# Kernel tuning notes

Hardware: AMD Instinct MI355X
Metric: run time of the kernel (lower is better)

Reference implementation:

```python
import jax, jax.numpy as jnp
import numpy as np

B, P, T, H, M = 32, 64, 256, 128, 16
MEAS_E, MOT_E = 64, 64
E = MEAS_E + MOT_E  # total_emb = 128
MAP_SIZE, MAP_EMB = 18, 128
ALPHA = 0.5  # soft-resampling alpha
OUT_DIM = 32 * 9 * 9  # encode output: conv1 stride2 18->9, conv2/3 stride1


def setup_inputs() -> dict:
    key = jax.random.key(0)
    ks = jax.random.split(key, 24)
    def g(i, shape, scale=0.05):
        return jax.random.normal(ks[i], shape, dtype=jnp.float32) * scale
    return {
        "map_in": jax.random.normal(ks[0], (B, 1, MAP_SIZE, MAP_SIZE), dtype=jnp.float32),
        "measurement_in": jax.random.normal(ks[1], (B, T, M), dtype=jnp.float32),
        "motion_in": jax.random.normal(ks[2], (B, T, 3), dtype=jnp.float32),
        "h0": jax.random.uniform(ks[3], (B * P, H), dtype=jnp.float32),
        "eps": jax.random.normal(ks[4], (T, B * P, H), dtype=jnp.float32),
        "u": jax.random.uniform(ks[5], (T, B, P), dtype=jnp.float32),
        "conv1_w": g(6, (16, 1, 5, 5)),
        "conv2_w": g(7, (32, 16, 3, 3)),
        "conv3_w": g(8, (32, 32, 3, 3)),
        "W_mapemb": g(9, (OUT_DIM, MAP_EMB)), "b_mapemb": jnp.zeros((MAP_EMB,), jnp.float32),
        "W_m2meas": g(10, (MAP_EMB, MEAS_E)), "b_m2meas": jnp.zeros((MEAS_E,), jnp.float32),
        "W_m2mot": g(11, (MAP_EMB, MOT_E)), "b_m2mot": jnp.zeros((MOT_E,), jnp.float32),
        "W_meas": g(12, (M, MEAS_E)), "b_meas": jnp.zeros((MEAS_E,), jnp.float32),
        "W_mot": g(13, (3, MOT_E)), "b_mot": jnp.zeros((MOT_E,), jnp.float32),
        "Wz": g(14, (H + E, H)), "bz": jnp.zeros((H,), jnp.float32),
        "Wr": g(15, (H + E, H)), "br": jnp.zeros((H,), jnp.float32),
        "Wn": g(16, (H + E, 2 * H)), "bn": jnp.zeros((2 * H,), jnp.float32),
        "Wo": g(17, (H + E, 1)), "bo": jnp.zeros((1,), jnp.float32),
        "W_label": g(18, (H, 3)), "b_label": jnp.zeros((3,), jnp.float32),
    }


def _encode(map_in, c1, c2, c3):
    # Conv -> ReLU -> BatchNorm(eval: identity w/ default stats) -> Dropout(eval: identity)
    dn = ("NCHW", "OIHW", "NCHW")
    x = jax.lax.conv_general_dilated(map_in, c1, (2, 2), [(2, 2), (2, 2)], dimension_numbers=dn)
    x = jax.nn.relu(x)
    x = jax.lax.conv_general_dilated(x, c2, (1, 1), [(1, 1), (1, 1)], dimension_numbers=dn)
    x = jax.nn.relu(x)
    x = jax.lax.conv_general_dilated(x, c3, (1, 1), [(1, 1), (1, 1)], dimension_numbers=dn)
    return jax.nn.relu(x)


def _pf_forward(map_in, measurement_in, motion_in, h0, eps, u,
                conv1_w, conv2_w, conv3_w,
                W_mapemb, b_mapemb, W_m2meas, b_m2meas, W_m2mot, b_m2mot,
                W_meas, b_meas, W_mot, b_mot,
                Wz, bz, Wr, br, Wn, bn, Wo, bo, W_label, b_label):
    relu = jax.nn.relu
    emb_map = _encode(map_in, conv1_w, conv2_w, conv3_w).reshape(B, -1)
    emb_map = relu(emb_map @ W_mapemb + b_mapemb)
    meas_map = relu(emb_map @ W_m2meas + b_m2meas)           # [B, MEAS_E]
    mot_map = relu(emb_map @ W_m2mot + b_m2mot)              # [B, MOT_E]
    emb_meas = relu(measurement_in @ W_meas + b_meas)        # [B, T, MEAS_E]
    emb_mot = relu(motion_in @ W_mot + b_mot)                # [B, T, MOT_E]
    embedding = jnp.concatenate([emb_meas * meas_map[:, None, :],
                                 emb_mot * mot_map[:, None, :]], axis=2)  # [B,T,E]
    embedding = jnp.tile(embedding, (P, 1, 1))               # [P*B, T, E] (repeat(pNumber,1,1))
    xs_emb = jnp.swapaxes(embedding, 0, 1)                   # [T, P*B, E]
    p0 = jnp.full((B * P, 1), np.log(1.0 / P), dtype=jnp.float32)
    inv_p = (1.0 - ALPHA) / P

    def cell(carry, step):
        h, p = carry                                         # [PB,H], [PB,1]
        x, ep, uu = step                                     # [PB,E], [PB,H], [B,P]
        hx = jnp.concatenate([h, x], axis=1)
        z = jax.nn.sigmoid(hx @ Wz + bz)
        r = jax.nn.sigmoid(hx @ Wr + br)
        n = jnp.concatenate([r * h, x], axis=1) @ Wn + bn
        mu, var = jnp.split(n, 2, axis=1)
        n = mu + ep * jax.nn.softplus(var)                   # reparameterize
        h1 = (1.0 - z) * n + z * h
        lp = jnp.concatenate([h1, x], axis=1) @ Wo + bo + p  # [PB,1] log obs-likelihood + prior
        lp = jax.nn.log_softmax(lp.reshape(P, B), axis=0)    # normalize over particles
        # soft resampling: q = alpha*w + (1-alpha)/P, inverse-CDF multinomial
        w = ALPHA * jnp.exp(lp) + inv_p                      # [P,B], sums to 1 over P
        cdf = jnp.cumsum(w.T, axis=1)                        # [B,P]
        idx = jax.vmap(lambda c, uv: jnp.searchsorted(c, uv * c[-1]))(cdf, uu)
        idx = jnp.clip(idx, 0, P - 1)                        # [B,P]
        idxT = idx.T                                         # [P,B]
        h_new = jnp.take_along_axis(h1.reshape(P, B, H), idxT[:, :, None], axis=0)
        p_g = jnp.take_along_axis(jnp.exp(lp), idxT, axis=0) # [P,B]
        p_new = jnp.log(ALPHA * p_g + inv_p)
        p_new = p_new - jax.scipy.special.logsumexp(p_new, axis=0, keepdims=True)
        h_new = h_new.reshape(B * P, H)
        p_new = p_new.reshape(B * P, 1)
        return (h_new, p_new), (h_new, p_new)

    _, (hs, ps) = jax.lax.scan(cell, (h0, p0), (xs_emb, eps, u))
    # hs: [T, PB, H]; hnn_dropout in eval mode -> identity
    y = jnp.sum(hs.reshape(T, P, B, H) * jnp.exp(ps.reshape(T, P, B, 1)), axis=1)  # [T,B,H]
    y_out = jax.nn.sigmoid(y @ W_label + b_label)            # sigmoid(xy)+sigmoid(h) == sigmoid(all)
    pf_out = jax.nn.sigmoid(hs @ W_label + b_label)          # [T, PB, 3]
    return y_out, pf_out


def reference(map_in, measurement_in, motion_in, h0, eps, u,
              conv1_w, conv2_w, conv3_w,
              W_mapemb, b_mapemb, W_m2meas, b_m2meas, W_m2mot, b_m2mot,
              W_meas, b_meas, W_mot, b_mot,
              Wz, bz, Wr, br, Wn, bn, Wo, bo, W_label, b_label):
    return _pf_forward(map_in, measurement_in, motion_in, h0, eps, u,
                       conv1_w, conv2_w, conv3_w,
                       W_mapemb, b_mapemb, W_m2meas, b_m2meas, W_m2mot, b_m2mot,
                       W_meas, b_meas, W_mot, b_mot,
                       Wz, bz, Wr, br, Wn, bn, Wo, bo, W_label, b_label)
```

## Files before the change

kernel.cpp:

```cpp
#include <hip/hip_runtime.h>
#include <cmath>

namespace {

constexpr int BB = 32, TT = 256, HH = 128;
constexpr int PB = 2048;
constexpr int WGPB = 8;
constexpr double INV_P = 0.0078125;
constexpr float LOG_P0 = -4.1588830833596715f;

__device__ __forceinline__ float sigf(float x) { return 1.f / (1.f + expf(-x)); }

__device__ __forceinline__ float ldc(const float* p) {
  return __hip_atomic_load(p, __ATOMIC_RELAXED, __HIP_MEMORY_SCOPE_AGENT);
}
__device__ __forceinline__ double ldc(const double* p) {
  return __hip_atomic_load(p, __ATOMIC_RELAXED, __HIP_MEMORY_SCOPE_AGENT);
}
__device__ __forceinline__ void stc(unsigned long long* p, unsigned long long v) {
  __hip_atomic_store(p, v, __ATOMIC_RELAXED, __HIP_MEMORY_SCOPE_AGENT);
}
__device__ __forceinline__ void stc(double* p, double v) {
  __hip_atomic_store(p, v, __ATOMIC_RELAXED, __HIP_MEMORY_SCOPE_AGENT);
}

__global__ void pack_kernel(const float* __restrict__ Wz, const float* __restrict__ Wr,
                            const float* __restrict__ Wn,
                            float* __restrict__ WzrH, float* __restrict__ WnH) {
  int tid = blockIdx.x * blockDim.x + threadIdx.x;
  int stride = gridDim.x * blockDim.x;
  for (int i = tid; i < 144 * 256; i += stride) {
    int k = i >> 8, c = i & 255;
    float vz = 0.f, vn = 0.f;
    if (k < 128) {
      vz = (c < 128) ? Wz[k * 128 + c] : Wr[k * 128 + (c - 128)];
      vn = Wn[k * 256 + c];
    }
    WzrH[i] = vz;
    WnH[i] = vn;
  }
}

__global__ __launch_bounds__(256) void encode_kernel(
    const float* __restrict__ map_in, const float* __restrict__ meas_in,
    const float* __restrict__ mot_in,
    const float* __restrict__ c1w, const float* __restrict__ c2w, const float* __restrict__ c3w,
    const float* __restrict__ Wme, const float* __restrict__ bme,
    const float* __restrict__ Wmm, const float* __restrict__ bmm,
    const float* __restrict__ Wmo, const float* __restrict__ bmo,
    const float* __restrict__ Wms, const float* __restrict__ bms,
    const float* __restrict__ Wmt, const float* __restrict__ bmt,
    float* __restrict__ emb) {
  const int b = blockIdx.x;
  const int tid = threadIdx.x;
  __shared__ float ml[324];
  __shared__ float o1[16 * 81];
  __shared__ float o2[32 * 81];
  __shared__ float o3[32 * 81];
  __shared__ float em[128];
  __shared__ float mm[64];
  __shared__ float mo[64];

  for (int i = tid; i < 324; i += 256) ml[i] = map_in[b * 324 + i];
  __syncthreads();
  for (int oid = tid; oid < 16 * 81; oid += 256) {
    int c = oid / 81, r = oid % 81, i = r / 9, j = r % 9;
    float acc = 0.f;
    for (int u = 0; u < 5; ++u) {
      int ii = 2 * i - 2 + u;
      if (ii < 0 || ii >= 18) continue;
      for (int v = 0; v < 5; ++v) {
        int jj = 2 * j - 2 + v;
        if (jj < 0 || jj >= 18) continue;
        acc += ml[ii * 18 + jj] * c1w[c * 25 + u * 5 + v];
      }
    }
    o1[oid] = fmaxf(acc, 0.f);
  }
  __syncthreads();
  for (int oid = tid; oid < 32 * 81; oid += 256) {
    int c = oid / 81, r = oid % 81, i = r / 9, j = r % 9;
    float acc = 0.f;
    for (int ci = 0; ci < 16; ++ci)
      for (int u = 0; u < 3; ++u) {
        int ii = i + u - 1;
        if (ii < 0 || ii >= 9) continue;
        for (int v = 0; v < 3; ++v) {
          int jj = j + v - 1;
          if (jj < 0 || jj >= 9) continue;
          acc += o1[ci * 81 + ii * 9 + jj] * c2w[((c * 16 + ci) * 3 + u) * 3 + v];
        }
      }
    o2[oid] = fmaxf(acc, 0.f);
  }
  __syncthreads();
  for (int oid = tid; oid < 32 * 81; oid += 256) {
    int c = oid / 81, r = oid % 81, i = r / 9, j = r % 9;
    float acc = 0.f;
    for (int ci = 0; ci < 32; ++ci)
      for (int u = 0; u < 3; ++u) {
        int ii = i + u - 1;
        if (ii < 0 || ii >= 9) continue;
        for (int v = 0; v < 3; ++v) {
          int jj = j + v - 1;
          if (jj < 0 || jj >= 9) continue;
          acc += o2[ci * 81 + ii * 9 + jj] * c3w[((c * 32 + ci) * 3 + u) * 3 + v];
        }
      }
    o3[oid] = fmaxf(acc, 0.f);
  }
  __syncthreads();
  if (tid < 128) {
    float acc = 0.f;
    for (int k = 0; k < 2592; ++k) acc += o3[k] * Wme[k * 128 + tid];
    em[tid] = fmaxf(acc + bme[tid], 0.f);
  }
  __syncthreads();
  if (tid < 64) {
    float a1 = 0.f, a2 = 0.f;
    for (int k = 0; k < 128; ++k) {
      a1 += em[k] * Wmm[k * 64 + tid];
      a2 += em[k] * Wmo[k * 64 + tid];
    }
    mm[tid] = fmaxf(a1 + bmm[tid], 0.f);
    mo[tid] = fmaxf(a2 + bmo[tid], 0.f);
  }
  __syncthreads();
  {
    int c = tid & 127;
    for (int t = tid >> 7; t < TT; t += 2) {
      float e;
      if (c < 64) {
        float acc = 0.f;
        for (int m = 0; m < 16; ++m) acc += meas_in[(size_t)(b * TT + t) * 16 + m] * Wms[m * 64 + c];
        e = fmaxf(acc + bms[c], 0.f) * mm[c];
      } else {
        int c2 = c - 64;
        float acc = 0.f;
        for (int m = 0; m < 3; ++m) acc += mot_in[(size_t)(b * TT + t) * 3 + m] * Wmt[m * 64 + c2];
        e = fmaxf(acc + bmt[c2], 0.f) * mo[c2];
      }
      emb[(size_t)(b * TT + t) * 128 + c] = e;
    }
  }
}

__global__ __launch_bounds__(128) void xdot_kernel(
    const float* __restrict__ emb, const float* __restrict__ Wz, const float* __restrict__ Wr,
    const float* __restrict__ Wn, const float* __restrict__ bz, const float* __restrict__ br,
    const float* __restrict__ bn, const float* __restrict__ Wo, const float* __restrict__ bo,
    float* __restrict__ xdot) {
  const int b = blockIdx.y;
  const int t0 = blockIdx.x * 8;
  __shared__ float xl[8][132];
  for (int i = threadIdx.x; i < 8 * 128; i += 128) {
    int r = i >> 7, d = i & 127;
    xl[r][d] = emb[(size_t)(b * TT + t0 + r) * 128 + d];
  }
  __syncthreads();
  const int c = threadIdx.x;
  float az[8] = {0}, ar[8] = {0}, an0[8] = {0}, an1[8] = {0};
  for (int k = 0; k < 128; ++k) {
    float wz = Wz[(128 + k) * 128 + c];
    float wr = Wr[(128 + k) * 128 + c];
    float w0 = Wn[(128 + k) * 256 + c];
    float w1 = Wn[(128 + k) * 256 + 128 + c];
#pragma unroll
    for (int r = 0; r < 8; ++r) {
      float x = xl[r][k];
      az[r] += x * wz; ar[r] += x * wr; an0[r] += x * w0; an1[r] += x * w1;
    }
  }
  for (int r = 0; r < 8; ++r) {
    size_t base = (size_t)((t0 + r) * BB + b) * 516;
    xdot[base + c] = az[r] + bz[c];
    xdot[base + 128 + c] = ar[r] + br[c];
    xdot[base + 256 + c] = an0[r] + bn[c];
    xdot[base + 384 + c] = an1[r] + bn[128 + c];
  }
  if (threadIdx.x < 8) {
    int r = threadIdx.x;
    float acc = 0.f;
    for (int k = 0; k < 128; ++k) acc += xl[r][k] * Wo[128 + k];
    xdot[(size_t)((t0 + r) * BB + b) * 516 + 512] = acc + bo[0];
  }
}

__device__ __forceinline__ void batch_barrier(unsigned* cnt, unsigned target) {
  asm volatile("s_waitcnt vmcnt(0)" ::: "memory");
  __syncthreads();
  if (threadIdx.x == 0) {
    __hip_atomic_fetch_add(cnt, 1u, __ATOMIC_RELAXED, __HIP_MEMORY_SCOPE_AGENT);
    unsigned v;
    do {
      __builtin_amdgcn_s_sleep(1);
      v = __hip_atomic_load(cnt, __ATOMIC_RELAXED, __HIP_MEMORY_SCOPE_AGENT);
    } while (v < target);
  }
  asm volatile("" ::: "memory");
  __syncthreads();
}

__global__ __attribute__((amdgpu_waves_per_eu(2, 2))) __launch_bounds__(512) void scan_kernel(
    const float* __restrict__ h0, const float* __restrict__ eps, const float* __restrict__ u_in,
    const float* __restrict__ Wo, const float* __restrict__ Wlab, const float* __restrict__ blab,
    const float* __restrict__ WzrH, const float* __restrict__ WnH, const float* __restrict__ xdot,
    float* __restrict__ h1buf, double* __restrict__ lpbuf, float* __restrict__ ybuf,
    float* __restrict__ pf_out, unsigned* __restrict__ counters) {
  const int tid = threadIdx.x;
  const int bid = blockIdx.x;
  const int b = bid & 31;
  const int wg = bid >> 5;

  __shared__ float part[8][8][256];
  __shared__ float hl[8][132];
  __shared__ float hT[128][8];
  __shared__ float rhl[8][132];
  __shared__ float rhT[128][8];
  __shared__ float xdl[520];
  __shared__ float wol[128];
  __shared__ float wll[384];
  __shared__ float bll[4];
  __shared__ double cdl[64];
  __shared__ double els[64];
  __shared__ float wnl[64];
  __shared__ int idxl[64];
  __shared__ float pl[8];

  unsigned* cnt = counters + b * 64;

  const int ks = tid >> 6;
  const int l = tid & 63;
  const int d_ = tid & 127;
  const int rp = tid >> 7;

  if (tid < 128) wol[tid] = Wo[tid];
  if (tid >= 128 && tid < 512) wll[tid - 128] = Wlab[tid - 128];
  if (tid < 4) bll[tid] = (tid < 3) ? blab[tid] : 0.f;
  if (tid < 8) pl[tid] = LOG_P0;
  {
    float v0 = h0[(size_t)((8 * wg + 2 * rp) * BB + b) * HH + d_];
    float v1 = h0[(size_t)((8 * wg + 2 * rp + 1) * BB + b) * HH + d_];
    hl[2 * rp][d_] = v0;
    hl[2 * rp + 1][d_] = v1;
    *(float2*)&hT[d_][2 * rp] = make_float2(v0, v1);
  }
  if (tid < 129)
    *(float4*)&xdl[tid * 4] = *(const float4*)&xdot[(size_t)(0 * BB + b) * 516 + tid * 4];

  float4 ep4 = make_float4(0.f, 0.f, 0.f, 0.f);
  if (l < 32)
    ep4 = *(const float4*)&eps[((size_t)0 * PB + (size_t)(8 * wg + ks) * BB + b) * HH + 4 * l];
  __syncthreads();

  for (int t = 0; t < TT; ++t) {
    const int par = t & 1;
    float z0, z1, z2, z3;

    {
      float a[8][4];
#pragma unroll
      for (int r = 0; r < 8; ++r)
#pragma unroll
        for (int j = 0; j < 4; ++j) a[r][j] = 0.f;
      const float* wp = WzrH + (size_t)(16 * ks) * 256 + 4 * l;
#pragma unroll
      for (int kk = 0; kk < 16; ++kk) {
        float4 w4 = *(const float4*)(wp + kk * 256);
        float4 hA = *(const float4*)&hT[16 * ks + kk][0];
        float4 hB = *(const float4*)&hT[16 * ks + kk][4];
        a[0][0] += hA.x * w4.x; a[0][1] += hA.x * w4.y; a[0][2] += hA.x * w4.z; a[0][3] += hA.x * w4.w;
        a[1][0] += hA.y * w4.x; a[1][1] += hA.y * w4.y; a[1][2] += hA.y * w4.z; a[1][3] += hA.y * w4.w;
        a[2][0] += hA.z * w4.x; a[2][1] += hA.z * w4.y; a[2][2] += hA.z * w4.z; a[2][3] += hA.z * w4.w;
        a[3][0] += hA.w * w4.x; a[3][1] += hA.w * w4.y; a[3][2] += hA.w * w4.z; a[3][3] += hA.w * w4.w;
        a[4][0] += hB.x * w4.x; a[4][1] += hB.x * w4.y; a[4][2] += hB.x * w4.z; a[4][3] += hB.x * w4.w;
        a[5][0] += hB.y * w4.x; a[5][1] += hB.y * w4.y; a[5][2] += hB.y * w4.z; a[5][3] += hB.y * w4.w;
        a[6][0] += hB.z * w4.x; a[6][1] += hB.z * w4.y; a[6][2] += hB.z * w4.z; a[6][3] += hB.z * w4.w;
        a[7][0] += hB.w * w4.x; a[7][1] += hB.w * w4.y; a[7][2] += hB.w * w4.z; a[7][3] += hB.w * w4.w;
      }
#pragma unroll
      for (int r = 0; r < 8; ++r)
        *(float4*)&part[ks][r][4 * l] = make_float4(a[r][0], a[r][1], a[r][2], a[r][3]);
    }
    __syncthreads();

    {
      int c0 = 4 * l;
      float s0 = 0.f, s1 = 0.f, s2 = 0.f, s3 = 0.f;
#pragma unroll
      for (int kq = 0; kq < 8; ++kq) {
        float4 p4 = *(const float4*)&part[kq][ks][c0];
        s0 += p4.x; s1 += p4.y; s2 += p4.z; s3 += p4.w;
      }
      s0 = sigf(s0 + xdl[c0 + 0]);
      s1 = sigf(s1 + xdl[c0 + 1]);
      s2 = sigf(s2 + xdl[c0 + 2]);
      s3 = sigf(s3 + xdl[c0 + 3]);
      if (l < 32) {
        z0 = s0; z1 = s1; z2 = s2; z3 = s3;
      } else {
        int cc = c0 - 128;
        float4 rh4;
        rh4.x = s0 * hl[ks][cc + 0];
        rh4.y = s1 * hl[ks][cc + 1];
        rh4.z = s2 * hl[ks][cc + 2];
        rh4.w = s3 * hl[ks][cc + 3];
        *(float4*)&rhl[ks][cc] = rh4;
      }
    }
    __syncthreads();

    {
      float t0v = rhl[2 * rp][d_];
      float t1v = rhl[2 * rp + 1][d_];
      *(float2*)&rhT[d_][2 * rp] = make_float2(t0v, t1v);
    }
    __syncthreads();

    {
      float a[8][4];
#pragma unroll
      for (int r = 0; r < 8; ++r)
#pragma unroll
        for (int j = 0; j < 4; ++j) a[r][j] = 0.f;
      const float* wp = WnH + (size_t)(16 * ks) * 256 + 4 * l;
#pragma unroll
      for (int kk = 0; kk < 16; ++kk) {
        float4 w4 = *(const float4*)(wp + kk * 256);
        float4 hA = *(const float4*)&rhT[16 * ks + kk][0];
        float4 hB = *(const float4*)&rhT[16 * ks + kk][4];
        a[0][0] += hA.x * w4.x; a[0][1] += hA.x * w4.y; a[0][2] += hA.x * w4.z; a[0][3] += hA.x * w4.w;
        a[1][0] += hA.y * w4.x; a[1][1] += hA.y * w4.y; a[1][2] += hA.y * w4.z; a[1][3] += hA.y * w4.w;
        a[2][0] += hA.z * w4.x; a[2][1] += hA.z * w4.y; a[2][2] += hA.z * w4.z; a[2][3] += hA.z * w4.w;
        a[3][0] += hA.w * w4.x; a[3][1] += hA.w * w4.y; a[3][2] += hA.w * w4.z; a[3][3] += hA.w * w4.w;
        a[4][0] += hB.x * w4.x; a[4][1] += hB.x * w4.y; a[4][2] += hB.x * w4.z; a[4][3] += hB.x * w4.w;
        a[5][0] += hB.y * w4.x; a[5][1] += hB.y * w4.y; a[5][2] += hB.y * w4.z; a[5][3] += hB.y * w4.w;
        a[6][0] += hB.z * w4.x; a[6][1] += hB.z * w4.y; a[6][2] += hB.z * w4.z; a[6][3] += hB.z * w4.w;
        a[7][0] += hB.w * w4.x; a[7][1] += hB.w * w4.y; a[7][2] += hB.w * w4.z; a[7][3] += hB.w * w4.w;
      }
#pragma unroll
      for (int r = 0; r < 8; ++r)
        *(float4*)&part[ks][r][4 * l] = make_float4(a[r][0], a[r][1], a[r][2], a[r][3]);
    }
    __syncthreads();

    {
      int c0 = 4 * l;
      float s0 = 0.f, s1 = 0.f, s2 = 0.f, s3 = 0.f;
#pragma unroll
      for (int kq = 0; kq < 8; ++kq) {
        float4 p4 = *(const float4*)&part[kq][ks][c0];
        s0 += p4.x; s1 += p4.y; s2 += p4.z; s3 += p4.w;
      }
      s0 += xdl[256 + c0 + 0];
      s1 += xdl[256 + c0 + 1];
      s2 += xdl[256 + c0 + 2];
      s3 += xdl[256 + c0 + 3];
      float va0 = __shfl(s0, l + 32);
      float va1 = __shfl(s1, l + 32);
      float va2 = __shfl(s2, l + 32);
      float va3 = __shfl(s3, l + 32);
      double lpacc = 0.0;
      if (l < 32) {
        float4 h4 = *(const float4*)&hl[ks][c0];
        float sp0 = fmaxf(va0, 0.f) + log1pf(expf(-fabsf(va0)));
        float sp1 = fmaxf(va1, 0.f) + log1pf(expf(-fabsf(va1)));
        float sp2 = fmaxf(va2, 0.f) + log1pf(expf(-fabsf(va2)));
        float sp3 = fmaxf(va3, 0.f) + log1pf(expf(-fabsf(va3)));
        float h10 = (1.f - z0) * (s0 + ep4.x * sp0) + z0 * h4.x;
        float h11 = (1.f - z1) * (s1 + ep4.y * sp1) + z1 * h4.y;
        float h12 = (1.f - z2) * (s2 + ep4.z * sp2) + z2 * h4.z;
        float h13 = (1.f - z3) * (s3 + ep4.w * sp3) + z3 * h4.w;
        union { unsigned long long u[2]; float f[4]; } pk;
        pk.f[0] = h10; pk.f[1] = h11; pk.f[2] = h12; pk.f[3] = h13;
        unsigned long long* dst = (unsigned long long*)
            &h1buf[((size_t)par * PB + (size_t)(8 * wg + ks) * BB + b) * HH + c0];
        stc(dst + 0, pk.u[0]);
        stc(dst + 1, pk.u[1]);
        lpacc = (double)h10 * (double)wol[c0 + 0] + (double)h11 * (double)wol[c0 + 1] +
                (double)h12 * (double)wol[c0 + 2] + (double)h13 * (double)wol[c0 + 3];
      }
#pragma unroll
      for (int o = 16; o > 0; o >>= 1) lpacc += __shfl_xor(lpacc, o);
      if (l == 0)
        stc(&lpbuf[par * PB + b * 64 + (8 * wg + ks)],
            lpacc + (double)xdl[512] + (double)pl[ks]);
    }

    const int tn = (t + 1 < TT) ? (t + 1) : t;
    float4 xpf = make_float4(0.f, 0.f, 0.f, 0.f);
    if (tid < 129) xpf = *(const float4*)&xdot[(size_t)(tn * BB + b) * 516 + tid * 4];
    if (l < 32)
      ep4 = *(const float4*)&eps[((size_t)tn * PB + (size_t)(8 * wg + ks) * BB + b) * HH + 4 * l];

    batch_barrier(cnt, (unsigned)(WGPB * (t + 1)));

    if (tid < 129) *(float4*)&xdl[tid * 4] = xpf;

    if (ks == 0) {
      double lp = ldc(&lpbuf[par * PB + b * 64 + l]);
      double m = lp;
#pragma unroll
      for (int o = 32; o > 0; o >>= 1) m = fmax(m, __shfl_xor(m, o));
      double e = exp(lp - m);
      double s = e;
#pragma unroll
      for (int o = 32; o > 0; o >>= 1) s += __shfl_xor(s, o);
      double lls = lp - m - log(s);
      double ee = exp(lls);
      els[l] = ee;
      double w = 0.5 * ee + INV_P;
      double run = w;
#pragma unroll
      for (int o = 1; o < 64; o <<= 1) {
        double v = __shfl_up(run, o);
        if (l >= o) run += v;
      }
      cdl[l] = run;
      double ctot = __shfl(run, 63);
      double uv = (double)u_in[((size_t)t * BB + b) * 64 + l] * ctot;
      int idx = 0;
#pragma unroll 8
      for (int i = 0; i < 64; ++i) idx += (cdl[i] < uv) ? 1 : 0;
      if (idx > 63) idx = 63;
      idxl[l] = idx;
      double pg = els[idx];
      double pnu = log(0.5 * pg + INV_P);
      double m2 = pnu;
#pragma unroll
      for (int o = 32; o > 0; o >>= 1) m2 = fmax(m2, __shfl_xor(m2, o));
      double s2 = exp(pnu - m2);
#pragma unroll
      for (int o = 32; o > 0; o >>= 1) s2 += __shfl_xor(s2, o);
      double pn = pnu - m2 - log(s2);
      wnl[l] = (float)exp(pn);
      if ((l >> 3) == wg) pl[l & 7] = (float)pn;
    }
    __syncthreads();

    {
      int a0i = idxl[8 * wg + 2 * rp];
      int a1i = idxl[8 * wg + 2 * rp + 1];
      float v0 = ldc(&h1buf[((size_t)par * PB + (size_t)a0i * BB + b) * HH + d_]);
      float v1 = ldc(&h1buf[((size_t)par * PB + (size_t)a1i * BB + b) * HH + d_]);
      hl[2 * rp][d_] = v0;
      hl[2 * rp + 1][d_] = v1;
      *(float2*)&hT[d_][2 * rp] = make_float2(v0, v1);
    }
    __syncthreads();

    {
      float ha = hl[ks][l], hb = hl[ks][l + 64];
      float p0 = ha * wll[l * 3 + 0] + hb * wll[(l + 64) * 3 + 0];
      float p1 = ha * wll[l * 3 + 1] + hb * wll[(l + 64) * 3 + 1];
      float p2 = ha * wll[l * 3 + 2] + hb * wll[(l + 64) * 3 + 2];
#pragma unroll
      for (int o = 32; o > 0; o >>= 1) {
        p0 += __shfl_xor(p0, o); p1 += __shfl_xor(p1, o); p2 += __shfl_xor(p2, o);
      }
      if (l == 0) {
        size_t base = ((size_t)t * PB + (size_t)(8 * wg + ks) * BB + b) * 3;
        pf_out[base + 0] = sigf(p0 + bll[0]);
        pf_out[base + 1] = sigf(p1 + bll[1]);
        pf_out[base + 2] = sigf(p2 + bll[2]);
      }
    }

    if (tid < 128) {
      float acc = 0.f;
#pragma unroll
      for (int r = 0; r < 8; ++r) acc += wnl[8 * wg + r] * hl[r][tid];
      atomicAdd(&ybuf[((size_t)t * BB + b) * HH + tid], acc);
    }
  }
}

__global__ __launch_bounds__(256) void yout_kernel(const float* __restrict__ ybuf,
                                                   const float* __restrict__ Wl,
                                                   const float* __restrict__ bl,
                                                   float* __restrict__ out) {
  __shared__ float wls[384];
  __shared__ float bls[3];
  int tid = threadIdx.x;
  for (int i = tid; i < 384; i += 256) wls[i] = Wl[i];
  if (tid < 3) bls[tid] = bl[tid];
  __syncthreads();
  int wv = tid >> 6, ln = tid & 63;
#pragma unroll
  for (int rr = 0; rr < 2; ++rr) {
    int rowi = blockIdx.x * 8 + wv * 2 + rr;
    float ya = ybuf[(size_t)rowi * 128 + ln];
    float yb = ybuf[(size_t)rowi * 128 + ln + 64];
    float p0 = ya * wls[ln * 3 + 0] + yb * wls[(ln + 64) * 3 + 0];
    float p1 = ya * wls[ln * 3 + 1] + yb * wls[(ln + 64) * 3 + 1];
    float p2 = ya * wls[ln * 3 + 2] + yb * wls[(ln + 64) * 3 + 2];
#pragma unroll
    for (int o = 32; o > 0; o >>= 1) {
      p0 += __shfl_xor(p0, o); p1 += __shfl_xor(p1, o); p2 += __shfl_xor(p2, o);
    }
    if (ln == 0) {
      out[(size_t)rowi * 3 + 0] = 1.f / (1.f + expf(-(p0 + bls[0])));
      out[(size_t)rowi * 3 + 1] = 1.f / (1.f + expf(-(p1 + bls[1])));
      out[(size_t)rowi * 3 + 2] = 1.f / (1.f + expf(-(p2 + bls[2])));
    }
  }
}

}

extern "C" void kernel_launch(void* const* d_in, const int* in_sizes, int n_in,
                              void* d_out, int out_size, void* d_ws, size_t ws_size,
                              hipStream_t stream) {
  const float* map_in = (const float*)d_in[0];
  const float* meas_in = (const float*)d_in[1];
  const float* mot_in = (const float*)d_in[2];
  const float* h0 = (const float*)d_in[3];
  const float* eps = (const float*)d_in[4];
  const float* u = (const float*)d_in[5];
  const float* c1w = (const float*)d_in[6];
  const float* c2w = (const float*)d_in[7];
  const float* c3w = (const float*)d_in[8];
  const float* Wme = (const float*)d_in[9];
  const float* bme = (const float*)d_in[10];
  const float* Wmm = (const float*)d_in[11];
  const float* bmm = (const float*)d_in[12];
  const float* Wmo = (const float*)d_in[13];
  const float* bmo = (const float*)d_in[14];
  const float* Wms = (const float*)d_in[15];
  const float* bms = (const float*)d_in[16];
  const float* Wmt = (const float*)d_in[17];
  const float* bmt = (const float*)d_in[18];
  const float* Wz = (const float*)d_in[19];
  const float* bz = (const float*)d_in[20];
  const float* Wr = (const float*)d_in[21];
  const float* br = (const float*)d_in[22];
  const float* Wn = (const float*)d_in[23];
  const float* bn = (const float*)d_in[24];
  const float* Wo = (const float*)d_in[25];
  const float* bo = (const float*)d_in[26];
  const float* Wl = (const float*)d_in[27];
  const float* bl = (const float*)d_in[28];

  char* ws = (char*)d_ws;
  unsigned* counters = (unsigned*)(ws + 0);
  float* WzrH = (float*)(ws + 8192);
  float* WnH = (float*)(ws + 155648);
  float* emb = (float*)(ws + 303104);
  float* xdot = (float*)(ws + 4497408);
  float* h1buf = (float*)(ws + 21405696);
  double* lpbuf = (double*)(ws + 23502848);
  float* ybuf = (float*)(ws + 23535616);
  if (ws_size < 27729920) return;

  float* out = (float*)d_out;
  float* pf_out = out + 24576;

  hipMemsetAsync(counters, 0, 8192, stream);
  hipMemsetAsync(ybuf, 0, 4194304, stream);
  hipLaunchKernelGGL(pack_kernel, dim3(144), dim3(256), 0, stream, Wz, Wr, Wn, WzrH, WnH);
  hipLaunchKernelGGL(encode_kernel, dim3(32), dim3(256), 0, stream, map_in, meas_in, mot_in,
                     c1w, c2w, c3w, Wme, bme, Wmm, bmm, Wmo, bmo, Wms, bms, Wmt, bmt, emb);
  hipLaunchKernelGGL(xdot_kernel, dim3(32, 32), dim3(128), 0, stream, emb, Wz, Wr, Wn, bz, br,
                     bn, Wo, bo, xdot);
  hipLaunchKernelGGL(scan_kernel, dim3(256), dim3(512), 0, stream, h0, eps, u, Wo, Wl, bl,
                     WzrH, WnH, xdot, h1buf, lpbuf, ybuf, pf_out, counters);
  hipLaunchKernelGGL(yout_kernel, dim3(1024), dim3(256), 0, stream, ybuf, Wl, bl, out);
}
```

Before: 5.392 ms.

## Split scan across 16 smaller workgroups per batch with 4 particles each

Changes the scan decomposition from 8 workgroups of 512 threads (8 particles each) to 16 workgroups of 256 threads (4 particles each) per batch, doubling the grid to 512 blocks. Each thread now covers 32 K-rows instead of 16 but keeps fewer accumulators, and block ids are remapped so the workgroups of one batch are contiguous. The aim is to spread the per-step recurrence across more CUs and shrink each block's critical path. In exchange the per-batch spin barrier now waits on twice as many participants, and the weight packing drops its unused zero-padded rows.

Result: slower. 7.803 ms (+44.7%).

```diff
diff --git a/kernel.cpp b/kernel.cpp
--- a/kernel.cpp
+++ b/kernel.cpp
@@ -5,7 +5,7 @@
 
 constexpr int BB = 32, TT = 256, HH = 128;
 constexpr int PB = 2048;
-constexpr int WGPB = 8;
+constexpr int WGPB = 16;
 constexpr double INV_P = 0.0078125;
 constexpr float LOG_P0 = -4.1588830833596715f;
 
@@ -29,15 +29,10 @@
                             float* __restrict__ WzrH, float* __restrict__ WnH) {
   int tid = blockIdx.x * blockDim.x + threadIdx.x;
   int stride = gridDim.x * blockDim.x;
-  for (int i = tid; i < 144 * 256; i += stride) {
+  for (int i = tid; i < 128 * 256; i += stride) {
     int k = i >> 8, c = i & 255;
-    float vz = 0.f, vn = 0.f;
-    if (k < 128) {
-      vz = (c < 128) ? Wz[k * 128 + c] : Wr[k * 128 + (c - 128)];
-      vn = Wn[k * 256 + c];
-    }
-    WzrH[i] = vz;
-    WnH[i] = vn;
+    WzrH[i] = (c < 128) ? Wz[k * 128 + c] : Wr[k * 128 + (c - 128)];
+    WnH[i] = Wn[k * 256 + c];
   }
 }
 
@@ -201,7 +196,7 @@
   __syncthreads();
 }
 
-__global__ __attribute__((amdgpu_waves_per_eu(2, 2))) __launch_bounds__(512) void scan_kernel(
+__global__ __launch_bounds__(256, 2) void scan_kernel(
     const float* __restrict__ h0, const float* __restrict__ eps, const float* __restrict__ u_in,
     const float* __restrict__ Wo, const float* __restrict__ Wlab, const float* __restrict__ blab,
     const float* __restrict__ WzrH, const float* __restrict__ WnH, const float* __restrict__ xdot,
@@ -209,14 +204,14 @@
     float* __restrict__ pf_out, unsigned* __restrict__ counters) {
   const int tid = threadIdx.x;
   const int bid = blockIdx.x;
-  const int b = bid & 31;
-  const int wg = bid >> 5;
-
-  __shared__ float part[8][8][256];
-  __shared__ float hl[8][132];
-  __shared__ float hT[128][8];
-  __shared__ float rhl[8][132];
-  __shared__ float rhT[128][8];
+  const int b = bid >> 4;
+  const int wg = bid & 15;
+
+  __shared__ __align__(16) float part[4][4][256];
+  __shared__ __align__(16) float hl[4][132];
+  __shared__ __align__(16) float hT[128][4];
+  __shared__ __align__(16) float rhl[4][132];
+  __shared__ __align__(16) float rhT[128][4];
   __shared__ float xdl[520];
   __shared__ float wol[128];
   __shared__ float wll[384];
@@ -225,7 +220,7 @@
   __shared__ double els[64];
   __shared__ float wnl[64];
   __shared__ int idxl[64];
-  __shared__ float pl[8];
+  __shared__ float pl[4];
 
   unsigned* cnt = counters + b * 64;
 
@@ -235,12 +230,11 @@
   const int rp = tid >> 7;
 
   if (tid < 128) wol[tid] = Wo[tid];
-  if (tid >= 128 && tid < 512) wll[tid - 128] = Wlab[tid - 128];
-  if (tid < 4) bll[tid] = (tid < 3) ? blab[tid] : 0.f;
-  if (tid < 8) pl[tid] = LOG_P0;
+  for (int i = tid; i < 384; i += 256) wll[i] = Wlab[i];
+  if (tid < 4) { bll[tid] = (tid < 3) ? blab[tid] : 0.f; pl[tid] = LOG_P0; }
   {
-    float v0 = h0[(size_t)((8 * wg + 2 * rp) * BB + b) * HH + d_];
-    float v1 = h0[(size_t)((8 * wg + 2 * rp + 1) * BB + b) * HH + d_];
+    float v0 = h0[(size_t)((4 * wg + 2 * rp) * BB + b) * HH + d_];
+    float v1 = h0[(size_t)((4 * wg + 2 * rp + 1) * BB + b) * HH + d_];
     hl[2 * rp][d_] = v0;
     hl[2 * rp + 1][d_] = v1;
     *(float2*)&hT[d_][2 * rp] = make_float2(v0, v1);
@@ -250,7 +244,7 @@
 
   float4 ep4 = make_float4(0.f, 0.f, 0.f, 0.f);
   if (l < 32)
-    ep4 = *(const float4*)&eps[((size_t)0 * PB + (size_t)(8 * wg + ks) * BB + b) * HH + 4 * l];
+    ep4 = *(const float4*)&eps[((size_t)0 * PB + (size_t)(4 * wg + ks) * BB + b) * HH + 4 * l];
   __syncthreads();
 
   for (int t = 0; t < TT; ++t) {
@@ -258,28 +252,23 @@
     float z0, z1, z2, z3;
 
     {
-      float a[8][4];
-#pragma unroll
-      for (int r = 0; r < 8; ++r)
+      float a[4][4];
+#pragma unroll
+      for (int r = 0; r < 4; ++r)
 #pragma unroll
         for (int j = 0; j < 4; ++j) a[r][j] = 0.f;
-      const float* wp = WzrH + (size_t)(16 * ks) * 256 + 4 * l;
-#pragma unroll
-      for (int kk = 0; kk < 16; ++kk) {
+      const float* wp = WzrH + (size_t)(32 * ks) * 256 + 4 * l;
+#pragma unroll
+      for (int kk = 0; kk < 32; ++kk) {
         float4 w4 = *(const float4*)(wp + kk * 256);
-        float4 hA = *(const float4*)&hT[16 * ks + kk][0];
-        float4 hB = *(const float4*)&hT[16 * ks + kk][4];
+        float4 hA = *(const float4*)&hT[32 * ks + kk][0];
         a[0][0] += hA.x * w4.x; a[0][1] += hA.x * w4.y; a[0][2] += hA.x * w4.z; a[0][3] += hA.x * w4.w;
         a[1][0] += hA.y * w4.x; a[1][1] += hA.y * w4.y; a[1][2] += hA.y * w4.z; a[1][3] += hA.y * w4.w;
         a[2][0] += hA.z * w4.x; a[2][1] += hA.z * w4.y; a[2][2] += hA.z * w4.z; a[2][3] += hA.z * w4.w;
         a[3][0] += hA.w * w4.x; a[3][1] += hA.w * w4.y; a[3][2] += hA.w * w4.z; a[3][3] += hA.w * w4.w;
-        a[4][0] += hB.x * w4.x; a[4][1] += hB.x * w4.y; a[4][2] += hB.x * w4.z; a[4][3] += hB.x * w4.w;
-        a[5][0] += hB.y * w4.x; a[5][1] += hB.y * w4.y; a[5][2] += hB.y * w4.z; a[5][3] += hB.y * w4.w;
-        a[6][0] += hB.z * w4.x; a[6][1] += hB.z * w4.y; a[6][2] += hB.z * w4.z; a[6][3] += hB.z * w4.w;
-        a[7][0] += hB.w * w4.x; a[7][1] += hB.w * w4.y; a[7][2] += hB.w * w4.z; a[7][3] += hB.w * w4.w;
-      }
-#pragma unroll
-      for (int r = 0; r < 8; ++r)
+      }
+#pragma unroll
+      for (int r = 0; r < 4; ++r)
         *(float4*)&part[ks][r][4 * l] = make_float4(a[r][0], a[r][1], a[r][2], a[r][3]);
     }
     __syncthreads();
@@ -288,7 +277,7 @@
       int c0 = 4 * l;
       float s0 = 0.f, s1 = 0.f, s2 = 0.f, s3 = 0.f;
 #pragma unroll
-      for (int kq = 0; kq < 8; ++kq) {
+      for (int kq = 0; kq < 4; ++kq) {
         float4 p4 = *(const float4*)&part[kq][ks][c0];
         s0 += p4.x; s1 += p4.y; s2 += p4.z; s3 += p4.w;
       }
@@ -318,28 +307,23 @@
     __syncthreads();
 
     {
-      float a[8][4];
-#pragma unroll
-      for (int r = 0; r < 8; ++r)
+      float a[4][4];
+#pragma unroll
+      for (int r = 0; r < 4; ++r)
 #pragma unroll
         for (int j = 0; j < 4; ++j) a[r][j] = 0.f;
-      const float* wp = WnH + (size_t)(16 * ks) * 256 + 4 * l;
-#pragma unroll
-      for (int kk = 0; kk < 16; ++kk) {
+      const float* wp = WnH + (size_t)(32 * ks) * 256 + 4 * l;
+#pragma unroll
+      for (int kk = 0; kk < 32; ++kk) {
         float4 w4 = *(const float4*)(wp + kk * 256);
-        float4 hA = *(const float4*)&rhT[16 * ks + kk][0];
-        float4 hB = *(const float4*)&rhT[16 * ks + kk][4];
+        float4 hA = *(const float4*)&rhT[32 * ks + kk][0];
         a[0][0] += hA.x * w4.x; a[0][1] += hA.x * w4.y; a[0][2] += hA.x * w4.z; a[0][3] += hA.x * w4.w;
         a[1][0] += hA.y * w4.x; a[1][1] += hA.y * w4.y; a[1][2] += hA.y * w4.z; a[1][3] += hA.y * w4.w;
         a[2][0] += hA.z * w4.x; a[2][1] += hA.z * w4.y; a[2][2] += hA.z * w4.z; a[2][3] += hA.z * w4.w;
         a[3][0] += hA.w * w4.x; a[3][1] += hA.w * w4.y; a[3][2] += hA.w * w4.z; a[3][3] += hA.w * w4.w;
-        a[4][0] += hB.x * w4.x; a[4][1] += hB.x * w4.y; a[4][2] += hB.x * w4.z; a[4][3] += hB.x * w4.w;
-        a[5][0] += hB.y * w4.x; a[5][1] += hB.y * w4.y; a[5][2] += hB.y * w4.z; a[5][3] += hB.y * w4.w;
-        a[6][0] += hB.z * w4.x; a[6][1] += hB.z * w4.y; a[6][2] += hB.z * w4.z; a[6][3] += hB.z * w4.w;
-        a[7][0] += hB.w * w4.x; a[7][1] += hB.w * w4.y; a[7][2] += hB.w * w4.z; a[7][3] += hB.w * w4.w;
-      }
-#pragma unroll
-      for (int r = 0; r < 8; ++r)
+      }
+#pragma unroll
+      for (int r = 0; r < 4; ++r)
         *(float4*)&part[ks][r][4 * l] = make_float4(a[r][0], a[r][1], a[r][2], a[r][3]);
     }
     __syncthreads();
@@ -348,7 +332,7 @@
       int c0 = 4 * l;
       float s0 = 0.f, s1 = 0.f, s2 = 0.f, s3 = 0.f;
 #pragma unroll
-      for (int kq = 0; kq < 8; ++kq) {
+      for (int kq = 0; kq < 4; ++kq) {
         float4 p4 = *(const float4*)&part[kq][ks][c0];
         s0 += p4.x; s1 += p4.y; s2 += p4.z; s3 += p4.w;
       }
@@ -374,7 +358,7 @@
         union { unsigned long long u[2]; float f[4]; } pk;
         pk.f[0] = h10; pk.f[1] = h11; pk.f[2] = h12; pk.f[3] = h13;
         unsigned long long* dst = (unsigned long long*)
-            &h1buf[((size_t)par * PB + (size_t)(8 * wg + ks) * BB + b) * HH + c0];
+            &h1buf[((size_t)par * PB + (size_t)(4 * wg + ks) * BB + b) * HH + c0];
         stc(dst + 0, pk.u[0]);
         stc(dst + 1, pk.u[1]);
         lpacc = (double)h10 * (double)wol[c0 + 0] + (double)h11 * (double)wol[c0 + 1] +
@@ -383,7 +367,7 @@
 #pragma unroll
       for (int o = 16; o > 0; o >>= 1) lpacc += __shfl_xor(lpacc, o);
       if (l == 0)
-        stc(&lpbuf[par * PB + b * 64 + (8 * wg + ks)],
+        stc(&lpbuf[par * PB + b * 64 + (4 * wg + ks)],
             lpacc + (double)xdl[512] + (double)pl[ks]);
     }
 
@@ -391,7 +375,7 @@
     float4 xpf = make_float4(0.f, 0.f, 0.f, 0.f);
     if (tid < 129) xpf = *(const float4*)&xdot[(size_t)(tn * BB + b) * 516 + tid * 4];
     if (l < 32)
-      ep4 = *(const float4*)&eps[((size_t)tn * PB + (size_t)(8 * wg + ks) * BB + b) * HH + 4 * l];
+      ep4 = *(const float4*)&eps[((size_t)tn * PB + (size_t)(4 * wg + ks) * BB + b) * HH + 4 * l];
 
     batch_barrier(cnt, (unsigned)(WGPB * (t + 1)));
 
@@ -434,13 +418,13 @@
       for (int o = 32; o > 0; o >>= 1) s2 += __shfl_xor(s2, o);
       double pn = pnu - m2 - log(s2);
       wnl[l] = (float)exp(pn);
-      if ((l >> 3) == wg) pl[l & 7] = (float)pn;
+      if ((l >> 2) == wg) pl[l & 3] = (float)pn;
     }
     __syncthreads();
 
     {
-      int a0i = idxl[8 * wg + 2 * rp];
-      int a1i = idxl[8 * wg + 2 * rp + 1];
+      int a0i = idxl[4 * wg + 2 * rp];
+      int a1i = idxl[4 * wg + 2 * rp + 1];
       float v0 = ldc(&h1buf[((size_t)par * PB + (size_t)a0i * BB + b) * HH + d_]);
       float v1 = ldc(&h1buf[((size_t)par * PB + (size_t)a1i * BB + b) * HH + d_]);
       hl[2 * rp][d_] = v0;
@@ -459,7 +443,7 @@
         p0 += __shfl_xor(p0, o); p1 += __shfl_xor(p1, o); p2 += __shfl_xor(p2, o);
       }
       if (l == 0) {
-        size_t base = ((size_t)t * PB + (size_t)(8 * wg + ks) * BB + b) * 3;
+        size_t base = ((size_t)t * PB + (size_t)(4 * wg + ks) * BB + b) * 3;
         pf_out[base + 0] = sigf(p0 + bll[0]);
         pf_out[base + 1] = sigf(p1 + bll[1]);
         pf_out[base + 2] = sigf(p2 + bll[2]);
@@ -469,7 +453,7 @@
     if (tid < 128) {
       float acc = 0.f;
 #pragma unroll
-      for (int r = 0; r < 8; ++r) acc += wnl[8 * wg + r] * hl[r][tid];
+      for (int r = 0; r < 4; ++r) acc += wnl[4 * wg + r] * hl[r][tid];
       atomicAdd(&ybuf[((size_t)t * BB + b) * HH + tid], acc);
     }
   }
@@ -544,25 +528,25 @@
   char* ws = (char*)d_ws;
   unsigned* counters = (unsigned*)(ws + 0);
   float* WzrH = (float*)(ws + 8192);
-  float* WnH = (float*)(ws + 155648);
-  float* emb = (float*)(ws + 303104);
-  float* xdot = (float*)(ws + 4497408);
-  float* h1buf = (float*)(ws + 21405696);
-  double* lpbuf = (double*)(ws + 23502848);
-  float* ybuf = (float*)(ws + 23535616);
-  if (ws_size < 27729920) return;
+  float* WnH = (float*)(ws + 139264);
+  float* emb = (float*)(ws + 270336);
+  float* xdot = (float*)(ws + 4464640);
+  float* h1buf = (float*)(ws + 21372928);
+  double* lpbuf = (double*)(ws + 23470080);
+  float* ybuf = (float*)(ws + 23502848);
+  if (ws_size < 27697152) return;
 
   float* out = (float*)d_out;
   float* pf_out = out + 24576;
 
   hipMemsetAsync(counters, 0, 8192, stream);
   hipMemsetAsync(ybuf, 0, 4194304, stream);
-  hipLaunchKernelGGL(pack_kernel, dim3(144), dim3(256), 0, stream, Wz, Wr, Wn, WzrH, WnH);
+  hipLaunchKernelGGL(pack_kernel, dim3(128), dim3(256), 0, stream, Wz, Wr, Wn, WzrH, WnH);
   hipLaunchKernelGGL(encode_kernel, dim3(32), dim3(256), 0, stream, map_in, meas_in, mot_in,
                      c1w, c2w, c3w, Wme, bme, Wmm, bmm, Wmo, bmo, Wms, bms, Wmt, bmt, emb);
   hipLaunchKernelGGL(xdot_kernel, dim3(32, 32), dim3(128), 0, stream, emb, Wz, Wr, Wn, bz, br,
                      bn, Wo, bo, xdot);
-  hipLaunchKernelGGL(scan_kernel, dim3(256), dim3(512), 0, stream, h0, eps, u, Wo, Wl, bl,
+  hipLaunchKernelGGL(scan_kernel, dim3(512), dim3(256), 0, stream, h0, eps, u, Wo, Wl, bl,
                      WzrH, WnH, xdot, h1buf, lpbuf, ybuf, pf_out, counters);
   hipLaunchKernelGGL(yout_kernel, dim3(1024), dim3(256), 0, stream, ybuf, Wl, bl, out);
 }
```

## Stage all parent hidden states in LDS and drop y atomics

Applied to the files above, without the earlier changes.

While wave 0 does the resampling math, the other waves now copy all 64 parent hidden rows for the batch into a new shared array, so the gather becomes an LDS read instead of scattered global loads. The weighted y reduction is computed per workgroup over a 16-column slice from that shared copy, with plain stores replacing atomicAdd, which also removes the ybuf memset. The log-domain softmax and renormalisation are simplified to direct ratios using shuffles, and the zero-padded packed weight rows are dropped. In exchange each workgroup loads 8x more h1 data per step and uses about 33KB more LDS, which may affect occupancy.

After: 5.752 ms. 6.7% more time.

```diff
diff --git a/kernel.cpp b/kernel.cpp
--- a/kernel.cpp
+++ b/kernel.cpp
@@ -17,6 +17,9 @@
 __device__ __forceinline__ double ldc(const double* p) {
   return __hip_atomic_load(p, __ATOMIC_RELAXED, __HIP_MEMORY_SCOPE_AGENT);
 }
+__device__ __forceinline__ unsigned long long ldc(const unsigned long long* p) {
+  return __hip_atomic_load(p, __ATOMIC_RELAXED, __HIP_MEMORY_SCOPE_AGENT);
+}
 __device__ __forceinline__ void stc(unsigned long long* p, unsigned long long v) {
   __hip_atomic_store(p, v, __ATOMIC_RELAXED, __HIP_MEMORY_SCOPE_AGENT);
 }
@@ -29,15 +32,10 @@
                             float* __restrict__ WzrH, float* __restrict__ WnH) {
   int tid = blockIdx.x * blockDim.x + threadIdx.x;
   int stride = gridDim.x * blockDim.x;
-  for (int i = tid; i < 144 * 256; i += stride) {
+  for (int i = tid; i < 128 * 256; i += stride) {
     int k = i >> 8, c = i & 255;
-    float vz = 0.f, vn = 0.f;
-    if (k < 128) {
-      vz = (c < 128) ? Wz[k * 128 + c] : Wr[k * 128 + (c - 128)];
-      vn = Wn[k * 256 + c];
-    }
-    WzrH[i] = vz;
-    WnH[i] = vn;
+    WzrH[i] = (c < 128) ? Wz[k * 128 + c] : Wr[k * 128 + (c - 128)];
+    WnH[i] = Wn[k * 256 + c];
   }
 }
 
@@ -217,12 +215,12 @@
   __shared__ float hT[128][8];
   __shared__ float rhl[8][132];
   __shared__ float rhT[128][8];
+  __shared__ float h1all[64][130];
   __shared__ float xdl[520];
   __shared__ float wol[128];
   __shared__ float wll[384];
   __shared__ float bll[4];
   __shared__ double cdl[64];
-  __shared__ double els[64];
   __shared__ float wnl[64];
   __shared__ int idxl[64];
   __shared__ float pl[8];
@@ -406,10 +404,8 @@
       double s = e;
 #pragma unroll
       for (int o = 32; o > 0; o >>= 1) s += __shfl_xor(s, o);
-      double lls = lp - m - log(s);
-      double ee = exp(lls);
-      els[l] = ee;
-      double w = 0.5 * ee + INV_P;
+      double els_v = e / s;
+      double w = 0.5 * els_v + INV_P;
       double run = w;
 #pragma unroll
       for (int o = 1; o < 64; o <<= 1) {
@@ -424,25 +420,28 @@
       for (int i = 0; i < 64; ++i) idx += (cdl[i] < uv) ? 1 : 0;
       if (idx > 63) idx = 63;
       idxl[l] = idx;
-      double pg = els[idx];
-      double pnu = log(0.5 * pg + INV_P);
-      double m2 = pnu;
-#pragma unroll
-      for (int o = 32; o > 0; o >>= 1) m2 = fmax(m2, __shfl_xor(m2, o));
-      double s2 = exp(pnu - m2);
-#pragma unroll
-      for (int o = 32; o > 0; o >>= 1) s2 += __shfl_xor(s2, o);
-      double pn = pnu - m2 - log(s2);
-      wnl[l] = (float)exp(pn);
-      if ((l >> 3) == wg) pl[l & 7] = (float)pn;
+      double pg = __shfl(els_v, idx);
+      double wg_ = 0.5 * pg + INV_P;
+      double S2 = wg_;
+#pragma unroll
+      for (int o = 32; o > 0; o >>= 1) S2 += __shfl_xor(S2, o);
+      wnl[l] = (float)(wg_ / S2);
+      if ((l >> 3) == wg) pl[l & 7] = (float)(log(wg_) - log(S2));
+    } else {
+      for (int i = tid - 64; i < 4096; i += 448) {
+        int a = i >> 6, dw = i & 63;
+        unsigned long long v = ldc((const unsigned long long*)
+            &h1buf[((size_t)par * PB + (size_t)a * BB + b) * HH + 2 * dw]);
+        *(unsigned long long*)&h1all[a][2 * dw] = v;
+      }
     }
     __syncthreads();
 
     {
       int a0i = idxl[8 * wg + 2 * rp];
       int a1i = idxl[8 * wg + 2 * rp + 1];
-      float v0 = ldc(&h1buf[((size_t)par * PB + (size_t)a0i * BB + b) * HH + d_]);
-      float v1 = ldc(&h1buf[((size_t)par * PB + (size_t)a1i * BB + b) * HH + d_]);
+      float v0 = h1all[a0i][d_];
+      float v1 = h1all[a1i][d_];
       hl[2 * rp][d_] = v0;
       hl[2 * rp + 1][d_] = v1;
       *(float2*)&hT[d_][2 * rp] = make_float2(v0, v1);
@@ -466,11 +465,12 @@
       }
     }
 
-    if (tid < 128) {
+    if (tid < 16) {
+      int dd = wg * 16 + tid;
       float acc = 0.f;
-#pragma unroll
-      for (int r = 0; r < 8; ++r) acc += wnl[8 * wg + r] * hl[r][tid];
-      atomicAdd(&ybuf[((size_t)t * BB + b) * HH + tid], acc);
+#pragma unroll 8
+      for (int j = 0; j < 64; ++j) acc += wnl[j] * h1all[idxl[j]][dd];
+      ybuf[((size_t)t * BB + b) * HH + dd] = acc;
     }
   }
 }
@@ -544,20 +544,19 @@
   char* ws = (char*)d_ws;
   unsigned* counters = (unsigned*)(ws + 0);
   float* WzrH = (float*)(ws + 8192);
-  float* WnH = (float*)(ws + 155648);
-  float* emb = (float*)(ws + 303104);
-  float* xdot = (float*)(ws + 4497408);
-  float* h1buf = (float*)(ws + 21405696);
-  double* lpbuf = (double*)(ws + 23502848);
-  float* ybuf = (float*)(ws + 23535616);
-  if (ws_size < 27729920) return;
+  float* WnH = (float*)(ws + 139264);
+  float* emb = (float*)(ws + 270336);
+  float* xdot = (float*)(ws + 4464640);
+  float* h1buf = (float*)(ws + 21372928);
+  double* lpbuf = (double*)(ws + 23470080);
+  float* ybuf = (float*)(ws + 23502848);
+  if (ws_size < 27697152) return;
 
   float* out = (float*)d_out;
   float* pf_out = out + 24576;
 
   hipMemsetAsync(counters, 0, 8192, stream);
-  hipMemsetAsync(ybuf, 0, 4194304, stream);
-  hipLaunchKernelGGL(pack_kernel, dim3(144), dim3(256), 0, stream, Wz, Wr, Wn, WzrH, WnH);
+  hipLaunchKernelGGL(pack_kernel, dim3(128), dim3(256), 0, stream, Wz, Wr, Wn, WzrH, WnH);
   hipLaunchKernelGGL(encode_kernel, dim3(32), dim3(256), 0, stream, map_in, meas_in, mot_in,
                      c1w, c2w, c3w, Wme, bme, Wmm, bmm, Wmo, bmo, Wms, bms, Wmt, bmt, emb);
   hipLaunchKernelGGL(xdot_kernel, dim3(32, 32), dim3(128), 0, stream, emb, Wz, Wr, Wn, bz, br,
```
